# Kernel tuning notes

Hardware: AMD Instinct MI355X
Metric: run time of the kernel (lower is better)

The kernel has to match this reference:

```python
import jax, jax.numpy as jnp
import numpy as np

B, Q, C, G = 16, 900, 1203, 100
CLS_W, BOX_W, HIER_W = 1.0, 5.0, 0.1
ALPHA, GAMMA = 0.25, 2.0


def setup_inputs() -> dict:
    key = jax.random.key(0)
    k = jax.random.split(key, 6)
    return {
        "logits": jax.random.normal(k[0], (B, Q, C), jnp.float32),
        "boxes": jax.random.uniform(k[1], (B, Q, 5), jnp.float32),
        "query_centers": jax.random.uniform(k[2], (B, Q, 2), jnp.float32),
        "gt_boxes": jax.random.uniform(k[3], (B, G, 5), jnp.float32),
        "gt_labels": jax.random.randint(k[4], (B, G), 0, C),
        "relation_matrix": jax.random.uniform(k[5], (C, C), jnp.float32),
    }


def _assign(qc, gboxes, glabels):
    # qc: [Q,2], gboxes: [G,5], glabels: [G]
    # Greedy one-to-one GT->query assignment, identical to the torch loop:
    # GTs processed in order of their min distance; each takes nearest unused query.
    d = jnp.linalg.norm(gboxes[:, None, :2] - qc[None, :, :], axis=-1)  # [G,Q]
    order = jnp.argsort(d.min(axis=1))  # [G]

    def step(used, g):
        dg = jnp.where(used, jnp.inf, d[g])
        q = jnp.argmin(dg)
        return used.at[q].set(True), q

    _, qs = jax.lax.scan(step, jnp.zeros((Q,), bool), order)  # [G] assigned query per ordered GT
    cls_t = jnp.zeros((Q, C), jnp.float32).at[qs, glabels[order]].set(1.0)
    box_t = jnp.zeros((Q, 5), jnp.float32).at[qs].set(gboxes[order])
    pos = jnp.zeros((Q,), bool).at[qs].set(True)
    return cls_t, box_t, pos


def reference(logits, boxes, query_centers, gt_boxes, gt_labels, relation_matrix):
    cls_t, box_t, pos = jax.vmap(_assign)(query_centers, gt_boxes, gt_labels)

    # sigmoid focal loss (mean over all B*Q*C elements)
    p = jax.nn.sigmoid(logits)
    ce = jnp.logaddexp(0.0, logits) - logits * cls_t  # stable BCE-with-logits
    p_t = p * cls_t + (1.0 - p) * (1.0 - cls_t)
    alpha_f = ALPHA * cls_t + (1.0 - ALPHA) * (1.0 - cls_t)
    cls_loss = jnp.mean(alpha_f * (1.0 - p_t) ** GAMMA * ce)

    # smooth-L1 on positive queries (beta=1, mean over selected elements)
    diff = boxes - box_t
    ad = jnp.abs(diff)
    sl1 = jnp.where(ad < 1.0, 0.5 * diff * diff, ad - 0.5)
    m = pos[..., None].astype(jnp.float32)  # [B,Q,1]
    box_loss = jnp.sum(sl1 * m) / jnp.maximum(jnp.sum(m) * 5.0, 1.0)

    # hierarchy laplacian loss
    probs = p.mean(axis=1)  # [B,C]
    lap = jnp.diag(relation_matrix.sum(axis=-1)) - relation_matrix
    hier_loss = jnp.einsum('bc,cd,bd->b', probs, lap, probs).mean()

    total = CLS_W * cls_loss + BOX_W * box_loss + HIER_W * hier_loss
    return total, cls_loss, box_loss, hier_loss
```

## Files before the change

### kernel.cpp

```cpp
#include <hip/hip_runtime.h>
#include <math.h>

#define BB 16
#define QQ 900
#define CC 1203
#define GG 100

constexpr int CT   = 5;
constexpr int QCH  = 20;
constexpr int QPC  = QQ / QCH;
constexpr int GBLK = BB;
constexpr int ABLK = CT * BB * QCH;

__device__ __forceinline__ void sig_sp(float x, float& p, float& sp) {
  float ax = fabsf(x);
  float e  = __expf(-ax);
  float r  = __builtin_amdgcn_rcpf(1.f + e);
  p  = (x >= 0.f) ? r : 1.f - r;
  sp = fmaxf(x, 0.f) + __logf(1.f + e);
}

__device__ __forceinline__ float dpp_min64(float x) {
  const int INFB = 0x7f800000;
  int xi = __float_as_int(x), t;
  t  = __builtin_amdgcn_update_dpp(INFB, xi, 0x111, 0xF, 0xF, false);
  xi = __float_as_int(fminf(__int_as_float(xi), __int_as_float(t)));
  t  = __builtin_amdgcn_update_dpp(INFB, xi, 0x112, 0xF, 0xF, false);
  xi = __float_as_int(fminf(__int_as_float(xi), __int_as_float(t)));
  t  = __builtin_amdgcn_update_dpp(INFB, xi, 0x114, 0xF, 0xF, false);
  xi = __float_as_int(fminf(__int_as_float(xi), __int_as_float(t)));
  t  = __builtin_amdgcn_update_dpp(INFB, xi, 0x118, 0xF, 0xF, false);
  xi = __float_as_int(fminf(__int_as_float(xi), __int_as_float(t)));
  t  = __builtin_amdgcn_update_dpp(INFB, xi, 0x142, 0xA, 0xF, false);
  xi = __float_as_int(fminf(__int_as_float(xi), __int_as_float(t)));
  t  = __builtin_amdgcn_update_dpp(INFB, xi, 0x143, 0xC, 0xF, false);
  xi = __float_as_int(fminf(__int_as_float(xi), __int_as_float(t)));
  return __int_as_float(xi);
}

__device__ __forceinline__ unsigned dpp_umin64(unsigned x) {
  unsigned t;
  t = (unsigned)__builtin_amdgcn_update_dpp((int)0xFFFFFFFFu, (int)x, 0x111, 0xF, 0xF, false);
  x = x < t ? x : t;
  t = (unsigned)__builtin_amdgcn_update_dpp((int)0xFFFFFFFFu, (int)x, 0x112, 0xF, 0xF, false);
  x = x < t ? x : t;
  t = (unsigned)__builtin_amdgcn_update_dpp((int)0xFFFFFFFFu, (int)x, 0x114, 0xF, 0xF, false);
  x = x < t ? x : t;
  t = (unsigned)__builtin_amdgcn_update_dpp((int)0xFFFFFFFFu, (int)x, 0x118, 0xF, 0xF, false);
  x = x < t ? x : t;
  t = (unsigned)__builtin_amdgcn_update_dpp((int)0xFFFFFFFFu, (int)x, 0x142, 0xA, 0xF, false);
  x = x < t ? x : t;
  t = (unsigned)__builtin_amdgcn_update_dpp((int)0xFFFFFFFFu, (int)x, 0x143, 0xC, 0xF, false);
  x = x < t ? x : t;
  return x;
}

__global__ __launch_bounds__(256) void fused_main(
    const float* __restrict__ logits, const float* __restrict__ boxes,
    const float* __restrict__ qcen,  const float* __restrict__ gtb,
    const int* __restrict__ gtl, float* __restrict__ probs_sum,
    double* __restrict__ accs)
{
  __shared__ float s_gx[GG], s_gy[GG], s_ming[GG];
  __shared__ float s_ogx[GG], s_ogy[GG];
  __shared__ int s_ord[GG], s_qs[GG];
  __shared__ double s_rd[8];

  const int bid  = blockIdx.x;
  const int tid  = threadIdx.x;
  const int lane = tid & 63;
  const int wv   = tid >> 6;
  const float FINF = __builtin_inff();

  if (bid < GBLK) {
    const int b = bid;
    const int cnt    = lane < 4 ? 15 : 14;
    const int qstart = lane < 4 ? lane * 15 : 60 + (lane - 4) * 14;
    float qx[15], qy[15];
    #pragma unroll
    for (int k = 0; k < 15; ++k) {
      int q = qstart + ((k < cnt) ? k : 0);
      float2 c2 = ((const float2*)qcen)[(size_t)b * QQ + q];
      qx[k] = (k < cnt) ? c2.x : FINF;
      qy[k] = (k < cnt) ? c2.y : 0.f;
    }
    if (tid < GG) {
      s_gx[tid] = gtb[((size_t)b * GG + tid) * 5 + 0];
      s_gy[tid] = gtb[((size_t)b * GG + tid) * 5 + 1];
    }
    __syncthreads();

    for (int g = wv * 25; g < (wv + 1) * 25; ++g) {
      float bx = s_gx[g], by = s_gy[g];
      float d[16];
      d[15] = FINF;
      #pragma unroll
      for (int k = 0; k < 15; ++k) {
        float dx = bx - qx[k], dy = by - qy[k];
        d[k] = fmaf(dy, dy, dx * dx);
      }
      #pragma unroll
      for (int s = 8; s >= 1; s >>= 1)
        #pragma unroll
        for (int k = 0; k < 8; ++k)
          if (k < s) d[k] = fminf(d[k], d[k + s]);
      float m = dpp_min64(d[0]);
      if (lane == 63) s_ming[g] = m;
    }
    __syncthreads();

    if (tid < GG) {
      float m = s_ming[tid];
      int r = 0;
      for (int j = 0; j < GG; ++j) {
        float mj = s_ming[j];
        r += (mj < m) || (mj == m && j < tid);
      }
      s_ord[r] = tid;
    }
    __syncthreads();
    if (tid < GG) {
      int g = s_ord[tid];
      s_ogx[tid] = s_gx[g];
      s_ogy[tid] = s_gy[g];
    }
    __syncthreads();

    float bx = s_ogx[0], by = s_ogy[0];
    for (int i = 0; i < GG; ++i) {
      int inext = (i + 1 < GG) ? i + 1 : i;
      float nbx = s_ogx[inext], nby = s_ogy[inext];
      unsigned p[16];
      p[15] = 0xFFFFFFFFu;
      #pragma unroll
      for (int k = 0; k < 15; ++k) {
        float dx = bx - qx[k], dy = by - qy[k];
        float dd = fmaf(dy, dy, dx * dx);
        p[k] = (__float_as_uint(dd) & 0xFFFFFFF0u) | (unsigned)k;
      }
      #pragma unroll
      for (int s = 8; s >= 1; s >>= 1)
        #pragma unroll
        for (int k = 0; k < 8; ++k)
          if (k < s) p[k] = p[k] < p[k + s] ? p[k] : p[k + s];
      unsigned wm = dpp_umin64(p[0]);
      wm = (unsigned)__builtin_amdgcn_readlane((int)wm, 63);
      unsigned long long ball = __ballot(p[0] == wm);
      int wl = __ffsll((long long)ball) - 1;
      int wk = (int)(wm & 15u);
      int qwin = (wl < 4 ? wl * 15 : 60 + (wl - 4) * 14) + wk;
      if (tid == 0) s_qs[i] = qwin;
      bool meW = (lane == wl);
      #pragma unroll
      for (int k = 0; k < 15; ++k)
        if (k == wk) qx[k] = meW ? FINF : qx[k];
      bx = nbx; by = nby;
    }
    __syncthreads();

    double dcls = 0.0, dbox = 0.0;
    if (tid < GG) {
      int g   = s_ord[tid];
      int q   = s_qs[tid];
      int lab = gtl[b * GG + g];
      float x = logits[((size_t)b * QQ + q) * CC + lab];
      float p, sp; sig_sp(x, p, sp);
      float omp = 1.f - p;
      dcls = (double)(0.25f * omp * omp * (sp - x)) -
             (double)(0.75f * p * p * sp);
      float bs = 0.f;
      #pragma unroll
      for (int j = 0; j < 5; ++j) {
        float diff = boxes[((size_t)b * QQ + q) * 5 + j] -
                     gtb[((size_t)b * GG + g) * 5 + j];
        float ad = fabsf(diff);
        bs += (ad < 1.f) ? 0.5f * diff * diff : ad - 0.5f;
      }
      dbox = (double)bs;
    }
    #pragma unroll
    for (int off = 32; off; off >>= 1) {
      dcls += __shfl_xor(dcls, off, 64);
      dbox += __shfl_xor(dbox, off, 64);
    }
    if (lane == 0) { s_rd[wv] = dcls; s_rd[4 + wv] = dbox; }
    __syncthreads();
    if (tid == 0) {
      atomicAdd(&accs[0], s_rd[0] + s_rd[1] + s_rd[2] + s_rd[3]);
      atomicAdd(&accs[1], s_rd[4] + s_rd[5] + s_rd[6] + s_rd[7]);
    }
  } else {
    int sid = bid - GBLK;
    int ct = sid % CT;
    int b  = (sid / CT) % BB;
    int qk = sid / (CT * BB);
    int c  = ct * 256 + tid;
    float s_sig = 0.f, s_foc = 0.f;
    if (c < CC) {
      const float* base = logits + ((size_t)b * QQ + (size_t)qk * QPC) * CC + c;
      for (int i0 = 0; i0 < QPC; i0 += 5) {
        float xs[5];
        #pragma unroll
        for (int u = 0; u < 5; ++u) xs[u] = base[(size_t)(i0 + u) * CC];
        #pragma unroll
        for (int u = 0; u < 5; ++u) {
          float p, sp; sig_sp(xs[u], p, sp);
          s_sig += p;
          s_foc += 0.75f * p * p * sp;
        }
      }
      atomicAdd(&probs_sum[b * CC + c], s_sig);
    }
    double v = (double)s_foc;
    #pragma unroll
    for (int off = 32; off; off >>= 1) v += __shfl_xor(v, off, 64);
    if (lane == 0) s_rd[wv] = v;
    __syncthreads();
    if (tid == 0) atomicAdd(&accs[0], s_rd[0] + s_rd[1] + s_rd[2] + s_rd[3]);
  }
}

__global__ __launch_bounds__(256) void hier_kernel(
    const float* __restrict__ Rm, const float* __restrict__ probs_sum,
    double* __restrict__ accs)
{
  __shared__ float s_x[BB * CC];
  __shared__ double s_rd[4];
  const int tid = threadIdx.x, lane = tid & 63, wv = tid >> 6;
  const float inv_q = 1.f / (float)QQ;
  constexpr int N4 = BB * CC / 4;
  const float4* src4 = (const float4*)probs_sum;
  for (int i = tid; i < N4; i += 256) {
    float4 v = src4[i];
    s_x[i * 4 + 0] = v.x * inv_q;
    s_x[i * 4 + 1] = v.y * inv_q;
    s_x[i * 4 + 2] = v.z * inv_q;
    s_x[i * 4 + 3] = v.w * inv_q;
  }
  __syncthreads();

  int c = blockIdx.x * 4 + wv;
  double part = 0.0;
  if (c < CC) {
    const float* row = Rm + (size_t)c * CC;
    float rs = 0.f, dot[BB];
    #pragma unroll
    for (int bb = 0; bb < BB; ++bb) dot[bb] = 0.f;
    for (int d = lane; d < CC; d += 64) {
      float r = row[d];
      rs += r;
      #pragma unroll
      for (int bb = 0; bb < BB; ++bb) dot[bb] = fmaf(r, s_x[bb * CC + d], dot[bb]);
    }
    #pragma unroll
    for (int off = 32; off; off >>= 1) {
      rs += __shfl_xor(rs, off, 64);
      #pragma unroll
      for (int bb = 0; bb < BB; ++bb) dot[bb] += __shfl_xor(dot[bb], off, 64);
    }
    if (lane == 0) {
      #pragma unroll
      for (int bb = 0; bb < BB; ++bb) {
        float xc = s_x[bb * CC + c];
        part += (double)xc * ((double)xc * (double)rs - (double)dot[bb]);
      }
    }
  }
  if (lane == 0) s_rd[wv] = part;
  __syncthreads();
  if (tid == 0) atomicAdd(&accs[2], s_rd[0] + s_rd[1] + s_rd[2] + s_rd[3]);
}

__global__ void finalize_kernel(const double* __restrict__ accs,
                                float* __restrict__ out)
{
  if (threadIdx.x == 0 && blockIdx.x == 0) {
    double cls  = accs[0] / (double)((size_t)BB * QQ * CC);
    double box  = accs[1] / 8000.0;
    double hier = accs[2] / (double)BB;
    double total = 1.0 * cls + 5.0 * box + 0.1 * hier;
    out[0] = (float)total;
    out[1] = (float)cls;
    out[2] = (float)box;
    out[3] = (float)hier;
  }
}

extern "C" void kernel_launch(void* const* d_in, const int* in_sizes, int n_in,
                              void* d_out, int out_size, void* d_ws, size_t ws_size,
                              hipStream_t stream) {
  const float* logits = (const float*)d_in[0];
  const float* boxes  = (const float*)d_in[1];
  const float* qcen   = (const float*)d_in[2];
  const float* gtb    = (const float*)d_in[3];
  const int*   gtl    = (const int*)d_in[4];
  const float* relm   = (const float*)d_in[5];

  float*  probs_sum = (float*)d_ws;
  double* accs      = (double*)((char*)d_ws + 80000);

  hipMemsetAsync(d_ws, 0, 80000 + 4 * sizeof(double), stream);

  fused_main<<<GBLK + ABLK, 256, 0, stream>>>(logits, boxes, qcen, gtb, gtl,
                                              probs_sum, accs);
  hier_kernel<<<(CC + 3) / 4, 256, 0, stream>>>(relm, probs_sum, accs);
  finalize_kernel<<<1, 64, 0, stream>>>(accs, (float*)d_out);
}
```

Before: 157.8 us.

## Reuse precomputed nearest query in greedy assignment, recompute only on conflict

The min-distance pass now also records which query is nearest to each GT (lane and slot). The serial greedy loop looks up that choice and redoes the full wave-wide argmin only when that query is already taken, tracked with a per-lane bitmask instead of writing infinity into the query coordinates. This is meant to shorten the serial critical path of the assignment blocks. It adds a readlane per step and relies on the quantised-key ordering matching the old argmin tie-breaking.

```diff
diff --git a/kernel.cpp b/kernel.cpp
--- a/kernel.cpp
+++ b/kernel.cpp
@@ -18,24 +18,6 @@
   float r  = __builtin_amdgcn_rcpf(1.f + e);
   p  = (x >= 0.f) ? r : 1.f - r;
   sp = fmaxf(x, 0.f) + __logf(1.f + e);
-}
-
-__device__ __forceinline__ float dpp_min64(float x) {
-  const int INFB = 0x7f800000;
-  int xi = __float_as_int(x), t;
-  t  = __builtin_amdgcn_update_dpp(INFB, xi, 0x111, 0xF, 0xF, false);
-  xi = __float_as_int(fminf(__int_as_float(xi), __int_as_float(t)));
-  t  = __builtin_amdgcn_update_dpp(INFB, xi, 0x112, 0xF, 0xF, false);
-  xi = __float_as_int(fminf(__int_as_float(xi), __int_as_float(t)));
-  t  = __builtin_amdgcn_update_dpp(INFB, xi, 0x114, 0xF, 0xF, false);
-  xi = __float_as_int(fminf(__int_as_float(xi), __int_as_float(t)));
-  t  = __builtin_amdgcn_update_dpp(INFB, xi, 0x118, 0xF, 0xF, false);
-  xi = __float_as_int(fminf(__int_as_float(xi), __int_as_float(t)));
-  t  = __builtin_amdgcn_update_dpp(INFB, xi, 0x142, 0xA, 0xF, false);
-  xi = __float_as_int(fminf(__int_as_float(xi), __int_as_float(t)));
-  t  = __builtin_amdgcn_update_dpp(INFB, xi, 0x143, 0xC, 0xF, false);
-  xi = __float_as_int(fminf(__int_as_float(xi), __int_as_float(t)));
-  return __int_as_float(xi);
 }
 
 __device__ __forceinline__ unsigned dpp_umin64(unsigned x) {
@@ -63,6 +45,7 @@
 {
   __shared__ float s_gx[GG], s_gy[GG], s_ming[GG];
   __shared__ float s_ogx[GG], s_ogy[GG];
+  __shared__ unsigned s_spec[GG], s_ospec[GG];
   __shared__ int s_ord[GG], s_qs[GG];
   __shared__ double s_rd[8];
 
@@ -92,20 +75,27 @@
 
     for (int g = wv * 25; g < (wv + 1) * 25; ++g) {
       float bx = s_gx[g], by = s_gy[g];
-      float d[16];
-      d[15] = FINF;
+      unsigned p[16];
+      p[15] = 0xFFFFFFFFu;
       #pragma unroll
       for (int k = 0; k < 15; ++k) {
         float dx = bx - qx[k], dy = by - qy[k];
-        d[k] = fmaf(dy, dy, dx * dx);
+        float dd = fmaf(dy, dy, dx * dx);
+        p[k] = (__float_as_uint(dd) & 0xFFFFFFF0u) | (unsigned)k;
       }
       #pragma unroll
       for (int s = 8; s >= 1; s >>= 1)
         #pragma unroll
         for (int k = 0; k < 8; ++k)
-          if (k < s) d[k] = fminf(d[k], d[k + s]);
-      float m = dpp_min64(d[0]);
-      if (lane == 63) s_ming[g] = m;
+          if (k < s) p[k] = p[k] < p[k + s] ? p[k] : p[k + s];
+      unsigned wm = dpp_umin64(p[0]);
+      wm = (unsigned)__builtin_amdgcn_readlane((int)wm, 63);
+      unsigned long long ball = __ballot(p[0] == wm);
+      int wl = __ffsll((long long)ball) - 1;
+      if (lane == 0) {
+        s_ming[g] = __uint_as_float(wm & 0xFFFFFFF0u);
+        s_spec[g] = (unsigned)((wl << 4) | (int)(wm & 15u));
+      }
     }
     __syncthreads();
 
@@ -121,40 +111,47 @@
     __syncthreads();
     if (tid < GG) {
       int g = s_ord[tid];
-      s_ogx[tid] = s_gx[g];
-      s_ogy[tid] = s_gy[g];
-    }
-    __syncthreads();
-
-    float bx = s_ogx[0], by = s_ogy[0];
+      s_ogx[tid]   = s_gx[g];
+      s_ogy[tid]   = s_gy[g];
+      s_ospec[tid] = s_spec[g];
+    }
+    __syncthreads();
+
+    unsigned sv0 = s_ospec[lane];
+    unsigned sv1 = s_ospec[(64 + lane) < GG ? (64 + lane) : (GG - 1)];
+
+    unsigned used = 0;
     for (int i = 0; i < GG; ++i) {
-      int inext = (i + 1 < GG) ? i + 1 : i;
-      float nbx = s_ogx[inext], nby = s_ogy[inext];
-      unsigned p[16];
-      p[15] = 0xFFFFFFFFu;
-      #pragma unroll
-      for (int k = 0; k < 15; ++k) {
-        float dx = bx - qx[k], dy = by - qy[k];
-        float dd = fmaf(dy, dy, dx * dx);
-        p[k] = (__float_as_uint(dd) & 0xFFFFFFF0u) | (unsigned)k;
-      }
-      #pragma unroll
-      for (int s = 8; s >= 1; s >>= 1)
-        #pragma unroll
-        for (int k = 0; k < 8; ++k)
-          if (k < s) p[k] = p[k] < p[k + s] ? p[k] : p[k + s];
-      unsigned wm = dpp_umin64(p[0]);
-      wm = (unsigned)__builtin_amdgcn_readlane((int)wm, 63);
-      unsigned long long ball = __ballot(p[0] == wm);
-      int wl = __ffsll((long long)ball) - 1;
-      int wk = (int)(wm & 15u);
+      unsigned spec = (unsigned)__builtin_amdgcn_readlane(
+          (int)(i < 64 ? sv0 : sv1), i & 63);
+      int wl = (int)(spec >> 4);
+      int wk = (int)(spec & 15u);
+      unsigned uwl = (unsigned)__builtin_amdgcn_readlane((int)used, wl);
+      if ((uwl >> wk) & 1u) {
+        float bx = s_ogx[i], by = s_ogy[i];
+        unsigned p[16];
+        p[15] = 0xFFFFFFFFu;
+        #pragma unroll
+        for (int k = 0; k < 15; ++k) {
+          float dx = bx - qx[k], dy = by - qy[k];
+          float dd = fmaf(dy, dy, dx * dx);
+          unsigned pk = (__float_as_uint(dd) & 0xFFFFFFF0u) | (unsigned)k;
+          p[k] = ((used >> k) & 1u) ? 0xFFFFFFFFu : pk;
+        }
+        #pragma unroll
+        for (int s = 8; s >= 1; s >>= 1)
+          #pragma unroll
+          for (int k = 0; k < 8; ++k)
+            if (k < s) p[k] = p[k] < p[k + s] ? p[k] : p[k + s];
+        unsigned wm = dpp_umin64(p[0]);
+        wm = (unsigned)__builtin_amdgcn_readlane((int)wm, 63);
+        unsigned long long ball = __ballot(p[0] == wm);
+        wl = __ffsll((long long)ball) - 1;
+        wk = (int)(wm & 15u);
+      }
       int qwin = (wl < 4 ? wl * 15 : 60 + (wl - 4) * 14) + wk;
+      if (lane == wl) used |= (1u << wk);
       if (tid == 0) s_qs[i] = qwin;
-      bool meW = (lane == wl);
-      #pragma unroll
-      for (int k = 0; k < 15; ++k)
-        if (k == wk) qx[k] = meW ? FINF : qx[k];
-      bx = nbx; by = nby;
     }
     __syncthreads();
 
```

Result: faster. 139.7 us (-11.5%).
